# Kernel tuning notes

Hardware: AMD Instinct MI355X
Metric: run time of the kernel (lower is better)

The kernel has to match this reference:

```python
import jax, jax.numpy as jnp
import numpy as np

D_MODEL = 2048
N_HEADS = 16
D_HEAD = D_MODEL // N_HEADS  # 128
SEQ = 2048
BATCH = 2


def setup_inputs() -> dict:
    key = jax.random.key(0)
    ks = jax.random.split(key, 6)
    x = jax.random.normal(ks[0], (SEQ, BATCH, D_MODEL), dtype=jnp.float32)
    # Realistic RoPE angles: theta[t, i] = t / 10000^(2i/d_head)
    inv_freq = 1.0 / (10000.0 ** (jnp.arange(0, D_HEAD, 2, dtype=jnp.float32) / D_HEAD))
    freqs = jnp.outer(jnp.arange(SEQ, dtype=jnp.float32), inv_freq)  # (SEQ, D_HEAD/2)
    s = 1.0 / np.sqrt(D_MODEL)
    W_qkv = jax.random.normal(ks[1], (3 * D_MODEL, D_MODEL), dtype=jnp.float32) * s
    b_qkv = jax.random.normal(ks[2], (3 * D_MODEL,), dtype=jnp.float32) * 0.01
    W_o = jax.random.normal(ks[3], (D_MODEL, D_MODEL), dtype=jnp.float32) * s
    b_o = jax.random.normal(ks[4], (D_MODEL,), dtype=jnp.float32) * 0.01
    return {"x": x, "freqs": freqs, "W_qkv": W_qkv, "b_qkv": b_qkv, "W_o": W_o, "b_o": b_o}


def _apply_rope(t, cos, sin):
    # t: (S, B, H, D); cos/sin: (S, 1, 1, D/2). Pairs are interleaved (even, odd),
    # matching torch.view_as_complex on reshape(..., -1, 2).
    tr = t.reshape(*t.shape[:-1], D_HEAD // 2, 2)
    a, b = tr[..., 0], tr[..., 1]
    out = jnp.stack([a * cos - b * sin, a * sin + b * cos], axis=-1)
    return out.reshape(t.shape)


def reference(x, freqs, W_qkv, b_qkv, W_o, b_o):
    S, B, _ = x.shape
    qkv = jnp.einsum('sbd,ed->sbe', x, W_qkv) + b_qkv  # (S, B, 3*D_MODEL)
    q, k, v = jnp.split(qkv, 3, axis=-1)
    q = q.reshape(S, B, N_HEADS, D_HEAD)
    k = k.reshape(S, B, N_HEADS, D_HEAD)
    v = v.reshape(S, B, N_HEADS, D_HEAD)
    cos = jnp.cos(freqs)[:, None, None, :]
    sin = jnp.sin(freqs)[:, None, None, :]
    q = _apply_rope(q, cos, sin)
    k = _apply_rope(k, cos, sin)
    # (S, B, H, D) -> (B, H, S, D)
    q = q.transpose(1, 2, 0, 3)
    k = k.transpose(1, 2, 0, 3)
    v = v.transpose(1, 2, 0, 3)
    scale = 1.0 / np.sqrt(D_HEAD).astype(np.float32)
    scores = jnp.einsum('bhqd,bhkd->bhqk', q, k) * scale  # (B, H, S, S)
    causal = jnp.tril(jnp.ones((S, S), dtype=bool))
    scores = jnp.where(causal, scores, jnp.finfo(scores.dtype).min)
    attn = jax.nn.softmax(scores, axis=-1)
    out = jnp.einsum('bhqk,bhkd->bhqd', attn, v)  # (B, H, S, D)
    out = out.transpose(2, 0, 1, 3).reshape(S, B, D_MODEL)
    return jnp.einsum('sbd,ed->sbe', out, W_o) + b_o
```

## Files before the change

kernel.cpp:

```cpp
#include <hip/hip_runtime.h>

#define D_MODEL 2048
#define N_HEADS 16
#define D_HEAD 128
#define SEQ 2048
#define BATCH 2
#define M_ROWS (SEQ*BATCH)
#define QKV_N  (3*D_MODEL)
#define ATTN_SCALE 0.08838834764831845f

typedef __attribute__((ext_vector_type(8))) short short8v;
typedef __attribute__((ext_vector_type(4))) float float4v;
typedef __attribute__((ext_vector_type(2))) unsigned int uint2v;
typedef __attribute__((ext_vector_type(4))) unsigned int uint4v;
typedef unsigned short u16;
typedef unsigned int   u32;

__device__ __forceinline__ u16 f32_bf16_rne(float f) {
    u32 u = __float_as_uint(f);
    return (u16)((u + 0x7FFFu + ((u >> 16) & 1u)) >> 16);
}
__device__ __forceinline__ float bf16_f32(u16 h) {
    return __uint_as_float(((u32)h) << 16);
}

__device__ __forceinline__ void gll16(const void* g, void* l) {
    __builtin_amdgcn_global_load_lds(
        (const __attribute__((address_space(1))) void*)g,
        (__attribute__((address_space(3))) void*)l, 16, 0, 0);
}

__global__ __launch_bounds__(256) void split_tiles(
    const float* __restrict__ src, u16* __restrict__ H, u16* __restrict__ L,
    const int R)
{
    const int kt = blockIdx.x, rt = blockIdx.y, t = threadIdx.x;
#pragma unroll
    for (int i = 0; i < 2; ++i) {
        const int s = i*256 + t;
        const int r = s >> 2, sub = s & 3;
        const float* p = src + (size_t)(rt*128 + r)*D_MODEL + kt*32 + sub*8;
        float4 v0 = ((const float4*)p)[0];
        float4 v1 = ((const float4*)p)[1];
        float vv[8] = {v0.x, v0.y, v0.z, v0.w, v1.x, v1.y, v1.z, v1.w};
        u16 hh[8], ll[8];
#pragma unroll
        for (int j = 0; j < 8; ++j) {
            hh[j] = f32_bf16_rne(vv[j]);
            ll[j] = f32_bf16_rne(vv[j] - bf16_f32(hh[j]));
        }
        const size_t off = ((size_t)kt*R + rt*128 + r)*32 + sub*8;
        *(uint4*)&H[off] = *(uint4*)hh;
        *(uint4*)&L[off] = *(uint4*)ll;
    }
}

__device__ __forceinline__ void ps_mainloop(
    const u16* __restrict__ Ah, const u16* __restrict__ Al,
    const u16* __restrict__ Bh, const u16* __restrict__ Bl,
    const int Mrows, const int Nrows, const int m0, const int n0,
    u16* lds, float4v (&acc)[4][4])
{
    const int t = threadIdx.x;
    const int lane = t & 63, wave = t >> 6;
    const int l16 = lane & 15, lg = lane >> 4;
    const int wm = wave >> 1, wn = wave & 1;
    u16* LAh = lds;          u16* LAl = lds + 4096;
    u16* LBh = lds + 8192;   u16* LBl = lds + 12288;
    const int ch0 = wave * 2;

    for (int kt = 0; kt < 64; ++kt) {
        __syncthreads();
        const size_t aoff = ((size_t)kt*Mrows + m0)*32;
        const size_t boff = ((size_t)kt*Nrows + n0)*32;
#pragma unroll
        for (int i = 0; i < 2; ++i) {
            const int ch = ch0 + i;
            const int go = ch*512 + lane*8;
            gll16(Ah + aoff + go, &LAh[ch*512]);
            gll16(Al + aoff + go, &LAl[ch*512]);
            gll16(Bh + boff + go, &LBh[ch*512]);
            gll16(Bl + boff + go, &LBl[ch*512]);
        }
        __syncthreads();

        short8v bh[4], bl[4];
#pragma unroll
        for (int fn = 0; fn < 4; ++fn) {
            const int rb = (wn*64 + fn*16 + l16)*32 + lg*8;
            bh[fn] = *(const short8v*)&LBh[rb];
            bl[fn] = *(const short8v*)&LBl[rb];
        }
#pragma unroll
        for (int fm = 0; fm < 4; ++fm) {
            const int ra = (wm*64 + fm*16 + l16)*32 + lg*8;
            short8v ah = *(const short8v*)&LAh[ra];
            short8v al = *(const short8v*)&LAl[ra];
#pragma unroll
            for (int fn = 0; fn < 4; ++fn) {
                acc[fm][fn] = __builtin_amdgcn_mfma_f32_16x16x32_bf16(ah, bh[fn], acc[fm][fn], 0,0,0);
                acc[fm][fn] = __builtin_amdgcn_mfma_f32_16x16x32_bf16(ah, bl[fn], acc[fm][fn], 0,0,0);
                acc[fm][fn] = __builtin_amdgcn_mfma_f32_16x16x32_bf16(al, bh[fn], acc[fm][fn], 0,0,0);
            }
        }
    }
}

__global__ __launch_bounds__(256, 3) void qkv_ps(
    const u16* __restrict__ Xh, const u16* __restrict__ Xl,
    const u16* __restrict__ Wh, const u16* __restrict__ Wl,
    const float* __restrict__ bias, const float* __restrict__ freqs,
    u16* __restrict__ Qh, u16* __restrict__ Ql,
    u16* __restrict__ Kh, u16* __restrict__ Kl,
    u16* __restrict__ Vh, u16* __restrict__ Vl)
{
    __shared__ u16 lds[16384];
    const int m0 = blockIdx.x*128, n0 = blockIdx.y*128;
    float4v acc[4][4];
#pragma unroll
    for (int i = 0; i < 4; ++i)
#pragma unroll
        for (int j = 0; j < 4; ++j)
#pragma unroll
            for (int r = 0; r < 4; ++r) acc[i][j][r] = 0.f;

    ps_mainloop(Xh, Xl, Wh, Wl, M_ROWS, QKV_N, m0, n0, lds, acc);

    const int t = threadIdx.x;
    const int lane = t & 63, wave = t >> 6;
    const int l16 = lane & 15, lg = lane >> 4;
    const int wm = wave >> 1, wn = wave & 1;
    const int sec = n0 >> 11;
    u16* __restrict__ hb = (sec == 0) ? Qh : ((sec == 1) ? Kh : Vh);
    u16* __restrict__ lb = (sec == 0) ? Ql : ((sec == 1) ? Kl : Vl);
#pragma unroll
    for (int fn = 0; fn < 4; ++fn) {
        const int n = n0 + wn*64 + fn*16 + l16;
        const float bn = bias[n];
        const int d = n & 127, hd = (n >> 7) & 15;
#pragma unroll
        for (int fm = 0; fm < 4; ++fm) {
#pragma unroll
            for (int r = 0; r < 4; ++r) {
                const int mrow = m0 + wm*64 + fm*16 + lg*4 + r;
                const int s = mrow >> 1, bb = mrow & 1;
                float v = acc[fm][fn][r] + bn;
                float outv;
                if (sec == 2) {
                    outv = v;
                } else {
                    float partner = __shfl_xor(v, 1, 64);
                    float fr = freqs[(size_t)s * 64 + (d >> 1)];
                    float sn, cs;
                    sincosf(fr, &sn, &cs);
                    outv = (n & 1) ? (partner*sn + v*cs) : (v*cs - partner*sn);
                    if (sec == 0) outv *= ATTN_SCALE;
                }
                size_t off = (((size_t)(bb*N_HEADS + hd) * SEQ) + s) * D_HEAD + d;
                u16 h = f32_bf16_rne(outv);
                hb[off] = h;
                lb[off] = f32_bf16_rne(outv - bf16_f32(h));
            }
        }
    }
}

__global__ __launch_bounds__(256, 3) void out_ps(
    const u16* __restrict__ Aph, const u16* __restrict__ Apl,
    const u16* __restrict__ Wh, const u16* __restrict__ Wl,
    const float* __restrict__ bias, float* __restrict__ Out)
{
    __shared__ u16 lds[16384];
    const int m0 = blockIdx.x*128, n0 = blockIdx.y*128;
    float4v acc[4][4];
#pragma unroll
    for (int i = 0; i < 4; ++i)
#pragma unroll
        for (int j = 0; j < 4; ++j)
#pragma unroll
            for (int r = 0; r < 4; ++r) acc[i][j][r] = 0.f;

    ps_mainloop(Aph, Apl, Wh, Wl, M_ROWS, D_MODEL, m0, n0, lds, acc);

    const int t = threadIdx.x;
    const int lane = t & 63, wave = t >> 6;
    const int l16 = lane & 15, lg = lane >> 4;
    const int wm = wave >> 1, wn = wave & 1;
#pragma unroll
    for (int fn = 0; fn < 4; ++fn) {
        const int n = n0 + wn*64 + fn*16 + l16;
        const float bn = bias[n];
#pragma unroll
        for (int fm = 0; fm < 4; ++fm) {
#pragma unroll
            for (int r = 0; r < 4; ++r) {
                const int mrow = m0 + wm*64 + fm*16 + lg*4 + r;
                Out[(size_t)mrow * D_MODEL + n] = acc[fm][fn][r] + bn;
            }
        }
    }
}

#define STAGE_SPLIT(vv, sH, sL)                                              \
    {                                                                        \
        _Pragma("unroll")                                                    \
        for (int q = 0; q < 4; ++q) {                                        \
            float4 v = vv[q];                                                \
            int off = ((half*2 + (q>>1))*128 + row)*8 + (q&1)*4;             \
            u16 h0 = f32_bf16_rne(v.x), h1 = f32_bf16_rne(v.y),              \
                h2 = f32_bf16_rne(v.z), h3 = f32_bf16_rne(v.w);              \
            ushort4 hv = make_ushort4(h0, h1, h2, h3);                       \
            ushort4 lv = make_ushort4(f32_bf16_rne(v.x - bf16_f32(h0)),      \
                                      f32_bf16_rne(v.y - bf16_f32(h1)),      \
                                      f32_bf16_rne(v.z - bf16_f32(h2)),      \
                                      f32_bf16_rne(v.w - bf16_f32(h3)));     \
            *(ushort4*)&sH[off] = hv;                                        \
            *(ushort4*)&sL[off] = lv;                                        \
        }                                                                    \
    }

#define GEMM_PROLOGUE()                                                      \
    __shared__ u16 sAh[4*128*8], sAl[4*128*8], sBh[4*128*8], sBl[4*128*8];   \
    const int t = threadIdx.x;                                               \
    const int m0 = blockIdx.x * 128, n0 = blockIdx.y * 128;                  \
    const int row = t >> 1, half = t & 1;                                    \
    const int lane = t & 63, wave = t >> 6;                                  \
    const int wm = wave >> 1, wn = wave & 1;                                 \
    const int l16 = lane & 15, lg = lane >> 4;                               \
    float4v acc[4][4];                                                       \
    _Pragma("unroll")                                                        \
    for (int i = 0; i < 4; ++i)                                              \
        _Pragma("unroll")                                                    \
        for (int j = 0; j < 4; ++j)                                          \
            _Pragma("unroll")                                                 \
            for (int r = 0; r < 4; ++r) acc[i][j][r] = 0.f;

#define GEMM_MAINLOOP(Aptr, Bptr)                                            \
    const float* Arow = (Aptr) + (size_t)(m0 + row) * D_MODEL + half*16;     \
    const float* Brow = (Bptr) + (size_t)(n0 + row) * D_MODEL + half*16;     \
    float4 pa[4], pb[4];                                                     \
    _Pragma("unroll")                                                        \
    for (int q = 0; q < 4; ++q) {                                            \
        pa[q] = ((const float4*)Arow)[q];                                    \
        pb[q] = ((const float4*)Brow)[q];                                    \
    }                                                                        \
    for (int kt = 0; kt < D_MODEL/32; ++kt) {                                \
        if (kt) __syncthreads();                                             \
        STAGE_SPLIT(pa, sAh, sAl);                                           \
        STAGE_SPLIT(pb, sBh, sBl);                                           \
        if (kt < D_MODEL/32 - 1) {                                           \
            Arow += 32; Brow += 32;                                          \
            _Pragma("unroll")                                                \
            for (int q = 0; q < 4; ++q) {                                    \
                pa[q] = ((const float4*)Arow)[q];                            \
                pb[q] = ((const float4*)Brow)[q];                            \
            }                                                                \
        }                                                                    \
        __syncthreads();                                                     \
        const int abase = lg*128 + wm*64 + l16;                              \
        const int bbase = lg*128 + wn*64 + l16;                              \
        short8v bh[4], bl[4];                                                \
        _Pragma("unroll")                                                    \
        for (int fn = 0; fn < 4; ++fn) {                                     \
            bh[fn] = ((const short8v*)sBh)[bbase + fn*16];                   \
            bl[fn] = ((const short8v*)sBl)[bbase + fn*16];                   \
        }                                                                    \
        _Pragma("unroll")                                                    \
        for (int fm = 0; fm < 4; ++fm) {                                     \
            short8v ah = ((const short8v*)sAh)[abase + fm*16];               \
            short8v al = ((const short8v*)sAl)[abase + fm*16];               \
            _Pragma("unroll")                                                \
            for (int fn = 0; fn < 4; ++fn) {                                 \
                acc[fm][fn] = __builtin_amdgcn_mfma_f32_16x16x32_bf16(       \
                    ah, bh[fn], acc[fm][fn], 0, 0, 0);                       \
                acc[fm][fn] = __builtin_amdgcn_mfma_f32_16x16x32_bf16(       \
                    ah, bl[fn], acc[fm][fn], 0, 0, 0);                       \
                acc[fm][fn] = __builtin_amdgcn_mfma_f32_16x16x32_bf16(       \
                    al, bh[fn], acc[fm][fn], 0, 0, 0);                       \
            }                                                                \
        }                                                                    \
    }

__global__ __launch_bounds__(256, 2) void qkv_rope_mfma(
    const float* __restrict__ X, const float* __restrict__ W,
    const float* __restrict__ bias, const float* __restrict__ freqs,
    u16* __restrict__ Qh, u16* __restrict__ Ql,
    u16* __restrict__ Kh, u16* __restrict__ Kl,
    u16* __restrict__ Vh, u16* __restrict__ Vl)
{
    GEMM_PROLOGUE();
    GEMM_MAINLOOP(X, W);
    const int sec = n0 >> 11;
    u16* __restrict__ hb = (sec == 0) ? Qh : ((sec == 1) ? Kh : Vh);
    u16* __restrict__ lb = (sec == 0) ? Ql : ((sec == 1) ? Kl : Vl);
#pragma unroll
    for (int fn = 0; fn < 4; ++fn) {
        const int n = n0 + wn*64 + fn*16 + l16;
        const float bn = bias[n];
        const int d = n & 127, hd = (n >> 7) & 15;
#pragma unroll
        for (int fm = 0; fm < 4; ++fm) {
#pragma unroll
            for (int r = 0; r < 4; ++r) {
                const int mrow = m0 + wm*64 + fm*16 + lg*4 + r;
                const int s = mrow >> 1, bb = mrow & 1;
                float v = acc[fm][fn][r] + bn;
                float outv;
                if (sec == 2) {
                    outv = v;
                } else {
                    float partner = __shfl_xor(v, 1, 64);
                    float fr = freqs[(size_t)s * 64 + (d >> 1)];
                    float sn, cs;
                    sincosf(fr, &sn, &cs);
                    outv = (n & 1) ? (partner*sn + v*cs) : (v*cs - partner*sn);
                    if (sec == 0) outv *= ATTN_SCALE;
                }
                size_t off = (((size_t)(bb*N_HEADS + hd) * SEQ) + s) * D_HEAD + d;
                u16 h = f32_bf16_rne(outv);
                hb[off] = h;
                lb[off] = f32_bf16_rne(outv - bf16_f32(h));
            }
        }
    }
}

__global__ __launch_bounds__(256, 2) void out_proj_mfma(
    const float* __restrict__ A, const float* __restrict__ W,
    const float* __restrict__ bias, float* __restrict__ Out)
{
    GEMM_PROLOGUE();
    GEMM_MAINLOOP(A, W);
#pragma unroll
    for (int fn = 0; fn < 4; ++fn) {
        const int n = n0 + wn*64 + fn*16 + l16;
        const float bn = bias[n];
#pragma unroll
        for (int fm = 0; fm < 4; ++fm) {
#pragma unroll
            for (int r = 0; r < 4; ++r) {
                const int mrow = m0 + wm*64 + fm*16 + lg*4 + r;
                Out[(size_t)mrow * D_MODEL + n] = acc[fm][fn][r] + bn;
            }
        }
    }
}

#define QH_O 0
#define QL_O 8192
#define KH_O 16384
#define KL_O 20480
#define VH_O 24576
#define VL_O 28672

#define PV_DB(DB)                                                            \
    {                                                                        \
        uint2v th0, th1, tl0, tl1;                                           \
        u32 aH = vbH + DB*1024, aL = vbL + DB*1024;                          \
        asm volatile("ds_read_b64_tr_b16 %0, %4\n\t"                         \
                     "ds_read_b64_tr_b16 %1, %4 offset:128\n\t"              \
                     "ds_read_b64_tr_b16 %2, %5\n\t"                         \
                     "ds_read_b64_tr_b16 %3, %5 offset:128\n\t"              \
                     "s_waitcnt lgkmcnt(0)"                                  \
                     : "=v"(th0), "=v"(th1), "=v"(tl0), "=v"(tl1)            \
                     : "v"(aH), "v"(aL));                                    \
        __builtin_amdgcn_sched_barrier(0);                                   \
        uint4v uh; uh.x = th0.x; uh.y = th0.y; uh.z = th1.x; uh.w = th1.y;   \
        uint4v ul; ul.x = tl0.x; ul.y = tl0.y; ul.z = tl1.x; ul.w = tl1.y;   \
        short8v vfh = __builtin_bit_cast(short8v, uh);                       \
        short8v vfl = __builtin_bit_cast(short8v, ul);                       \
        o[DB] = __builtin_amdgcn_mfma_f32_16x16x32_bf16(vfh, pfh, o[DB], 0,0,0); \
        o[DB] = __builtin_amdgcn_mfma_f32_16x16x32_bf16(vfh, pfl, o[DB], 0,0,0); \
        o[DB] = __builtin_amdgcn_mfma_f32_16x16x32_bf16(vfl, pfh, o[DB], 0,0,0); \
    }

template<int MODE>
__global__ __launch_bounds__(256, 2) void attn_mfma_t(
    const u16* __restrict__ Qh_g, const u16* __restrict__ Ql_g,
    const u16* __restrict__ Kh_g, const u16* __restrict__ Kl_g,
    const u16* __restrict__ Vh_g, const u16* __restrict__ Vl_g,
    float* __restrict__ Op, u16* __restrict__ AH, u16* __restrict__ AL)
{
    __shared__ __align__(16) u16 lds[32768];

    const int t = threadIdx.x;
    const int lane = t & 63, wave = t >> 6;
    const int l16 = lane & 15, lg = lane >> 4;

    const int bid = blockIdx.x;
    const int bh = (bid & 7) * 4 + ((bid >> 3) >> 4);
    const int pairid = (bid >> 3) & 15;
    const size_t ho = (size_t)bh * SEQ * D_HEAD;

    const int skv = t >> 3;
    const int sdb = t & 7;

    const u32 ldsb = (u32)(uintptr_t)lds;
    const u32 vbH = ldsb + VH_O*2 + lg*256 + l16*8;
    const u32 vbL = ldsb + VL_O*2 + lg*256 + l16*8;

    for (int pass = 0; pass < 2; ++pass) {
        const int qb = pass ? (31 - pairid) : pairid;
        const int q0 = qb * 64;
        __syncthreads();
#pragma unroll
        for (int i = 0; i < 2; ++i) {
            int task = i*256 + t;
            int qr = task >> 3, db = task & 7;
            size_t gsrc = ho + (size_t)(q0 + qr)*128 + db*16;
            uint4 h0 = *(const uint4*)(Qh_g + gsrc);
            uint4 h1 = *(const uint4*)(Qh_g + gsrc + 8);
            uint4 L0 = *(const uint4*)(Ql_g + gsrc);
            uint4 L1 = *(const uint4*)(Ql_g + gsrc + 8);
            *(uint4*)&lds[QH_O + ((db*2  )*64 + qr)*8] = h0;
            *(uint4*)&lds[QH_O + ((db*2+1)*64 + qr)*8] = h1;
            *(uint4*)&lds[QL_O + ((db*2  )*64 + qr)*8] = L0;
            *(uint4*)&lds[QL_O + ((db*2+1)*64 + qr)*8] = L1;
        }
        __syncthreads();
        short8v qfh[4], qfl[4];
#pragma unroll
        for (int c = 0; c < 4; ++c) {
            int g = c*4 + lg;
            qfh[c] = *(const short8v*)&lds[QH_O + (g*64 + wave*16 + l16)*8];
            qfl[c] = *(const short8v*)&lds[QL_O + (g*64 + wave*16 + l16)*8];
        }

        float4v o[8];
#pragma unroll
        for (int db = 0; db < 8; ++db)
#pragma unroll
            for (int r = 0; r < 4; ++r) o[db][r] = 0.f;
        float m_s = -1e30f, l_s = 0.f;

        const int jjmax = 2*qb + 1;
        for (int jj = 0; jj <= jjmax; ++jj) {
            const int kv0 = jj * 32;
            __syncthreads();
            {
                size_t gk = ho + (size_t)(kv0 + skv)*128 + sdb*16;
                uint4 kh0 = *(const uint4*)(Kh_g + gk);
                uint4 kh1 = *(const uint4*)(Kh_g + gk + 8);
                uint4 kl0 = *(const uint4*)(Kl_g + gk);
                uint4 kl1 = *(const uint4*)(Kl_g + gk + 8);
                uint4 vh0 = *(const uint4*)(Vh_g + gk);
                uint4 vh1 = *(const uint4*)(Vh_g + gk + 8);
                uint4 vl0 = *(const uint4*)(Vl_g + gk);
                uint4 vl1 = *(const uint4*)(Vl_g + gk + 8);
                const int k7 = skv & 7;
                const int g0 = sdb*2, g1 = sdb*2 + 1;
                *(uint4*)&lds[KH_O + skv*128 + ((g0^k7)<<3)] = kh0;
                *(uint4*)&lds[KH_O + skv*128 + ((g1^k7)<<3)] = kh1;
                *(uint4*)&lds[KL_O + skv*128 + ((g0^k7)<<3)] = kl0;
                *(uint4*)&lds[KL_O + skv*128 + ((g1^k7)<<3)] = kl1;
                const int vreg = (sdb*8 + (skv>>2))*64 + (skv&3)*16;
                *(uint4*)&lds[VH_O + vreg]     = vh0;
                *(uint4*)&lds[VH_O + vreg + 8] = vh1;
                *(uint4*)&lds[VL_O + vreg]     = vl0;
                *(uint4*)&lds[VL_O + vreg + 8] = vl1;
            }
            __syncthreads();

            float4v s0 = {0.f,0.f,0.f,0.f}, s1 = {0.f,0.f,0.f,0.f};
#pragma unroll
            for (int c = 0; c < 4; ++c) {
                const int x0 = ((c*4 + lg) ^ (l16 & 7)) << 3;
                short8v kh0 = *(const short8v*)&lds[KH_O + l16*128 + x0];
                short8v kl0 = *(const short8v*)&lds[KL_O + l16*128 + x0];
                short8v kh1 = *(const short8v*)&lds[KH_O + (16+l16)*128 + x0];
                short8v kl1 = *(const short8v*)&lds[KL_O + (16+l16)*128 + x0];
                s0 = __builtin_amdgcn_mfma_f32_16x16x32_bf16(kh0, qfh[c], s0, 0,0,0);
                s0 = __builtin_amdgcn_mfma_f32_16x16x32_bf16(kh0, qfl[c], s0, 0,0,0);
                s0 = __builtin_amdgcn_mfma_f32_16x16x32_bf16(kl0, qfh[c], s0, 0,0,0);
                s1 = __builtin_amdgcn_mfma_f32_16x16x32_bf16(kh1, qfh[c], s1, 0,0,0);
                s1 = __builtin_amdgcn_mfma_f32_16x16x32_bf16(kh1, qfl[c], s1, 0,0,0);
                s1 = __builtin_amdgcn_mfma_f32_16x16x32_bf16(kl1, qfh[c], s1, 0,0,0);
            }

            const int qg = q0 + wave*16 + l16;
            if (jj >= 2*qb) {
#pragma unroll
                for (int r = 0; r < 4; ++r) {
                    if (kv0 + lg*4 + r > qg)      s0[r] = -1e30f;
                    if (kv0 + 16 + lg*4 + r > qg) s1[r] = -1e30f;
                }
            }

            float mx = fmaxf(fmaxf(fmaxf(s0[0], s0[1]), fmaxf(s0[2], s0[3])),
                             fmaxf(fmaxf(s1[0], s1[1]), fmaxf(s1[2], s1[3])));
            mx = fmaxf(mx, __shfl_xor(mx, 16, 64));
            mx = fmaxf(mx, __shfl_xor(mx, 32, 64));
            const float newm = fmaxf(m_s, mx);
            const float alpha = __expf(m_s - newm);
            m_s = newm;
            float pA[4], pB[4];
#pragma unroll
            for (int r = 0; r < 4; ++r) {
                pA[r] = __expf(s0[r] - newm);
                pB[r] = __expf(s1[r] - newm);
            }
            float rs = (pA[0]+pA[1]+pA[2]+pA[3]) + (pB[0]+pB[1]+pB[2]+pB[3]);
            rs += __shfl_xor(rs, 16, 64);
            rs += __shfl_xor(rs, 32, 64);
            l_s = l_s * alpha + rs;
#pragma unroll
            for (int db = 0; db < 8; ++db)
#pragma unroll
                for (int r = 0; r < 4; ++r) o[db][r] *= alpha;

            u16 ph[8], pl[8];
#pragma unroll
            for (int r = 0; r < 4; ++r) {
                float T1 = __shfl_xor(pA[r], 32, 64);
                float T2 = __shfl_xor(pB[r], 32, 64);
                float pv = (lg==0) ? T1 : (lg==1) ? pA[r] : (lg==2) ? pB[r] : T2;
                float Rv = __shfl_xor(pv, 16, 64);
                float X  = (lg==0) ? pA[r] : (lg==1) ? Rv : (lg==2) ? T2 : Rv;
                float Y  = (lg==0) ? Rv    : (lg==1) ? T1 : (lg==2) ? Rv : pB[r];
                u16 hx = f32_bf16_rne(X);
                ph[r]   = hx; pl[r]   = f32_bf16_rne(X - bf16_f32(hx));
                u16 hy = f32_bf16_rne(Y);
                ph[4+r] = hy; pl[4+r] = f32_bf16_rne(Y - bf16_f32(hy));
            }
            short8v pfh, pfl;
            pfh[0]=(short)ph[0]; pfh[1]=(short)ph[1]; pfh[2]=(short)ph[2]; pfh[3]=(short)ph[3];
            pfh[4]=(short)ph[4]; pfh[5]=(short)ph[5]; pfh[6]=(short)ph[6]; pfh[7]=(short)ph[7];
            pfl[0]=(short)pl[0]; pfl[1]=(short)pl[1]; pfl[2]=(short)pl[2]; pfl[3]=(short)pl[3];
            pfl[4]=(short)pl[4]; pfl[5]=(short)pl[5]; pfl[6]=(short)pl[6]; pfl[7]=(short)pl[7];

            PV_DB(0) PV_DB(1) PV_DB(2) PV_DB(3)
            PV_DB(4) PV_DB(5) PV_DB(6) PV_DB(7)
        }

        const int bb = bh >> 4, hh = bh & 15;
        const float inv = 1.0f / l_s;
        const int s_row = q0 + wave*16 + l16;
        if constexpr (MODE == 0) {
            float* orow = Op + (size_t)(s_row*BATCH + bb) * D_MODEL + hh*128;
#pragma unroll
            for (int tile = 0; tile < 8; ++tile) {
                float4 w = make_float4(o[tile][0]*inv, o[tile][1]*inv,
                                       o[tile][2]*inv, o[tile][3]*inv);
                *(float4*)(orow + tile*16 + lg*4) = w;
            }
        } else {
            const int m = s_row*BATCH + bb;
#pragma unroll
            for (int tile = 0; tile < 8; ++tile) {
                const int kt = hh*4 + (tile >> 1);
                const size_t off = ((size_t)kt*M_ROWS + m)*32 + (tile & 1)*16 + lg*4;
                u16 hh4[4], ll4[4];
#pragma unroll
                for (int r = 0; r < 4; ++r) {
                    float w = o[tile][r]*inv;
                    hh4[r] = f32_bf16_rne(w);
                    ll4[r] = f32_bf16_rne(w - bf16_f32(hh4[r]));
                }
                *(ushort4*)&AH[off] = make_ushort4(hh4[0], hh4[1], hh4[2], hh4[3]);
                *(ushort4*)&AL[off] = make_ushort4(ll4[0], ll4[1], ll4[2], ll4[3]);
            }
        }
    }
}

extern "C" void kernel_launch(void* const* d_in, const int* in_sizes, int n_in,
                              void* d_out, int out_size, void* d_ws, size_t ws_size,
                              hipStream_t stream) {
    const float* x      = (const float*)d_in[0];
    const float* freqs  = (const float*)d_in[1];
    const float* W_qkv  = (const float*)d_in[2];
    const float* b_qkv  = (const float*)d_in[3];
    const float* W_o    = (const float*)d_in[4];
    const float* b_o    = (const float*)d_in[5];
    float* out = (float*)d_out;

    const size_t PX = (size_t)M_ROWS * D_MODEL;
    const size_t PW = (size_t)QKV_N  * D_MODEL;
    const size_t PO = (size_t)D_MODEL* D_MODEL;
    u16* ws16 = (u16*)d_ws;

    if (ws_size >= (10*PX + 2*PW + 2*PO) * sizeof(u16)) {
        u16* Xh  = ws16;            u16* Xl  = Xh  + PX;
        u16* Wqh = Xl + PX;         u16* Wql = Wqh + PW;
        u16* Woh = Wql + PW;        u16* Wol = Woh + PO;
        u16* Qh  = Wol + PO;        u16* Ql  = Qh + PX;
        u16* Kh  = Ql + PX;         u16* Kl  = Kh + PX;
        u16* Vh  = Kl + PX;         u16* Vl  = Vh + PX;
        u16* Ahp = Vl + PX;         u16* Alp = Ahp + PX;

        split_tiles<<<dim3(64, M_ROWS/128), 256, 0, stream>>>(x,     Xh,  Xl,  M_ROWS);
        split_tiles<<<dim3(64, QKV_N/128),  256, 0, stream>>>(W_qkv, Wqh, Wql, QKV_N);
        split_tiles<<<dim3(64, D_MODEL/128),256, 0, stream>>>(W_o,   Woh, Wol, D_MODEL);
        qkv_ps<<<dim3(M_ROWS/128, QKV_N/128), 256, 0, stream>>>(
            Xh, Xl, Wqh, Wql, b_qkv, freqs, Qh, Ql, Kh, Kl, Vh, Vl);
        attn_mfma_t<1><<<dim3(512), 256, 0, stream>>>(
            Qh, Ql, Kh, Kl, Vh, Vl, nullptr, Ahp, Alp);
        out_ps<<<dim3(M_ROWS/128, D_MODEL/128), 256, 0, stream>>>(
            Ahp, Alp, Woh, Wol, b_o, out);
    } else {
        u16 *Qh = ws16,       *Ql = ws16 + PX,   *Kh = ws16 + 2*PX,
            *Kl = ws16 + 3*PX, *Vh = ws16 + 4*PX, *Vl = ws16 + 5*PX;
        float* attn = (float*)(ws16 + 6*PX);

        qkv_rope_mfma<<<dim3(M_ROWS/128, QKV_N/128), 256, 0, stream>>>(
            x, W_qkv, b_qkv, freqs, Qh, Ql, Kh, Kl, Vh, Vl);
        attn_mfma_t<0><<<dim3(512), 256, 0, stream>>>(
            Qh, Ql, Kh, Kl, Vh, Vl, attn, nullptr, nullptr);
        out_proj_mfma<<<dim3(M_ROWS/128, D_MODEL/128), 256, 0, stream>>>(
            attn, W_o, b_o, out);
    }
}
```

Before: 730.4 us.

## Double-buffer LDS in split-bf16 GEMMs and prefetch K/V tiles in attention

The shared GEMM mainloop now uses two LDS buffers. It issues the global-to-LDS loads for the next k-tile before computing the current one, replacing two barriers per iteration with one vmcnt wait and barrier at the end. The attention kernel prefetches the next K/V block into registers while the current block is written to LDS and computed. LDS per GEMM block doubles and launch bounds drop from 3 to 2 blocks per CU, trading occupancy for overlap. The fallback fp32-staging kernels and the small-workspace path are removed.

```diff
diff --git a/kernel.cpp b/kernel.cpp
--- a/kernel.cpp
+++ b/kernel.cpp
@@ -65,48 +65,74 @@
     const int lane = t & 63, wave = t >> 6;
     const int l16 = lane & 15, lg = lane >> 4;
     const int wm = wave >> 1, wn = wave & 1;
-    u16* LAh = lds;          u16* LAl = lds + 4096;
-    u16* LBh = lds + 8192;   u16* LBl = lds + 12288;
     const int ch0 = wave * 2;
 
-    for (int kt = 0; kt < 64; ++kt) {
-        __syncthreads();
-        const size_t aoff = ((size_t)kt*Mrows + m0)*32;
-        const size_t boff = ((size_t)kt*Nrows + n0)*32;
+    {
+        const size_t aoff = (size_t)m0 * 32;
+        const size_t boff = (size_t)n0 * 32;
 #pragma unroll
         for (int i = 0; i < 2; ++i) {
             const int ch = ch0 + i;
             const int go = ch*512 + lane*8;
-            gll16(Ah + aoff + go, &LAh[ch*512]);
-            gll16(Al + aoff + go, &LAl[ch*512]);
-            gll16(Bh + boff + go, &LBh[ch*512]);
-            gll16(Bl + boff + go, &LBl[ch*512]);
-        }
-        __syncthreads();
-
-        short8v bh[4], bl[4];
+            gll16(Ah + aoff + go, &lds[        ch*512]);
+            gll16(Al + aoff + go, &lds[ 4096 + ch*512]);
+            gll16(Bh + boff + go, &lds[ 8192 + ch*512]);
+            gll16(Bl + boff + go, &lds[12288 + ch*512]);
+        }
+    }
+    asm volatile("s_waitcnt vmcnt(0)" ::: "memory");
+    __builtin_amdgcn_s_barrier();
+    __builtin_amdgcn_sched_barrier(0);
+
+    int cur = 0;
+    for (int kt = 0; kt < 64; ++kt) {
+        if (kt < 63) {
+            u16* dst = lds + (cur^1)*16384;
+            const size_t aoff = ((size_t)(kt+1)*Mrows + m0)*32;
+            const size_t boff = ((size_t)(kt+1)*Nrows + n0)*32;
+#pragma unroll
+            for (int i = 0; i < 2; ++i) {
+                const int ch = ch0 + i;
+                const int go = ch*512 + lane*8;
+                gll16(Ah + aoff + go, &dst[        ch*512]);
+                gll16(Al + aoff + go, &dst[ 4096 + ch*512]);
+                gll16(Bh + boff + go, &dst[ 8192 + ch*512]);
+                gll16(Bl + boff + go, &dst[12288 + ch*512]);
+            }
+        }
+        const u16* src = lds + cur*16384;
+        short8v bhf[4], blf[4], ahf[4], alf[4];
 #pragma unroll
         for (int fn = 0; fn < 4; ++fn) {
             const int rb = (wn*64 + fn*16 + l16)*32 + lg*8;
-            bh[fn] = *(const short8v*)&LBh[rb];
-            bl[fn] = *(const short8v*)&LBl[rb];
+            bhf[fn] = *(const short8v*)&src[ 8192 + rb];
+            blf[fn] = *(const short8v*)&src[12288 + rb];
         }
 #pragma unroll
         for (int fm = 0; fm < 4; ++fm) {
             const int ra = (wm*64 + fm*16 + l16)*32 + lg*8;
-            short8v ah = *(const short8v*)&LAh[ra];
-            short8v al = *(const short8v*)&LAl[ra];
+            ahf[fm] = *(const short8v*)&src[       ra];
+            alf[fm] = *(const short8v*)&src[4096 + ra];
+        }
+        asm volatile("s_waitcnt lgkmcnt(0)" ::: "memory");
+        __builtin_amdgcn_sched_barrier(0);
+#pragma unroll
+        for (int fm = 0; fm < 4; ++fm) {
 #pragma unroll
             for (int fn = 0; fn < 4; ++fn) {
-                acc[fm][fn] = __builtin_amdgcn_mfma_f32_16x16x32_bf16(ah, bh[fn], acc[fm][fn], 0,0,0);
-                acc[fm][fn] = __builtin_amdgcn_mfma_f32_16x16x32_bf16(ah, bl[fn], acc[fm][fn], 0,0,0);
-                acc[fm][fn] = __builtin_amdgcn_mfma_f32_16x16x32_bf16(al, bh[fn], acc[fm][fn], 0,0,0);
-            }
-        }
-    }
-}
-
-__global__ __launch_bounds__(256, 3) void qkv_ps(
+                acc[fm][fn] = __builtin_amdgcn_mfma_f32_16x16x32_bf16(ahf[fm], bhf[fn], acc[fm][fn], 0,0,0);
+                acc[fm][fn] = __builtin_amdgcn_mfma_f32_16x16x32_bf16(ahf[fm], blf[fn], acc[fm][fn], 0,0,0);
+                acc[fm][fn] = __builtin_amdgcn_mfma_f32_16x16x32_bf16(alf[fm], bhf[fn], acc[fm][fn], 0,0,0);
+            }
+        }
+        asm volatile("s_waitcnt vmcnt(0)" ::: "memory");
+        __builtin_amdgcn_s_barrier();
+        __builtin_amdgcn_sched_barrier(0);
+        cur ^= 1;
+    }
+}
+
+__global__ __launch_bounds__(256, 2) void qkv_ps(
     const u16* __restrict__ Xh, const u16* __restrict__ Xl,
     const u16* __restrict__ Wh, const u16* __restrict__ Wl,
     const float* __restrict__ bias, const float* __restrict__ freqs,
@@ -114,7 +140,7 @@
     u16* __restrict__ Kh, u16* __restrict__ Kl,
     u16* __restrict__ Vh, u16* __restrict__ Vl)
 {
-    __shared__ u16 lds[16384];
+    __shared__ u16 lds[32768];
     const int m0 = blockIdx.x*128, n0 = blockIdx.y*128;
     float4v acc[4][4];
 #pragma unroll
@@ -165,12 +191,12 @@
     }
 }
 
-__global__ __launch_bounds__(256, 3) void out_ps(
+__global__ __launch_bounds__(256, 2) void out_ps(
     const u16* __restrict__ Aph, const u16* __restrict__ Apl,
     const u16* __restrict__ Wh, const u16* __restrict__ Wl,
     const float* __restrict__ bias, float* __restrict__ Out)
 {
-    __shared__ u16 lds[16384];
+    __shared__ u16 lds[32768];
     const int m0 = blockIdx.x*128, n0 = blockIdx.y*128;
     float4v acc[4][4];
 #pragma unroll
@@ -186,151 +212,6 @@
     const int lane = t & 63, wave = t >> 6;
     const int l16 = lane & 15, lg = lane >> 4;
     const int wm = wave >> 1, wn = wave & 1;
-#pragma unroll
-    for (int fn = 0; fn < 4; ++fn) {
-        const int n = n0 + wn*64 + fn*16 + l16;
-        const float bn = bias[n];
-#pragma unroll
-        for (int fm = 0; fm < 4; ++fm) {
-#pragma unroll
-            for (int r = 0; r < 4; ++r) {
-                const int mrow = m0 + wm*64 + fm*16 + lg*4 + r;
-                Out[(size_t)mrow * D_MODEL + n] = acc[fm][fn][r] + bn;
-            }
-        }
-    }
-}
-
-#define STAGE_SPLIT(vv, sH, sL)                                              \
-    {                                                                        \
-        _Pragma("unroll")                                                    \
-        for (int q = 0; q < 4; ++q) {                                        \
-            float4 v = vv[q];                                                \
-            int off = ((half*2 + (q>>1))*128 + row)*8 + (q&1)*4;             \
-            u16 h0 = f32_bf16_rne(v.x), h1 = f32_bf16_rne(v.y),              \
-                h2 = f32_bf16_rne(v.z), h3 = f32_bf16_rne(v.w);              \
-            ushort4 hv = make_ushort4(h0, h1, h2, h3);                       \
-            ushort4 lv = make_ushort4(f32_bf16_rne(v.x - bf16_f32(h0)),      \
-                                      f32_bf16_rne(v.y - bf16_f32(h1)),      \
-                                      f32_bf16_rne(v.z - bf16_f32(h2)),      \
-                                      f32_bf16_rne(v.w - bf16_f32(h3)));     \
-            *(ushort4*)&sH[off] = hv;                                        \
-            *(ushort4*)&sL[off] = lv;                                        \
-        }                                                                    \
-    }
-
-#define GEMM_PROLOGUE()                                                      \
-    __shared__ u16 sAh[4*128*8], sAl[4*128*8], sBh[4*128*8], sBl[4*128*8];   \
-    const int t = threadIdx.x;                                               \
-    const int m0 = blockIdx.x * 128, n0 = blockIdx.y * 128;                  \
-    const int row = t >> 1, half = t & 1;                                    \
-    const int lane = t & 63, wave = t >> 6;                                  \
-    const int wm = wave >> 1, wn = wave & 1;                                 \
-    const int l16 = lane & 15, lg = lane >> 4;                               \
-    float4v acc[4][4];                                                       \
-    _Pragma("unroll")                                                        \
-    for (int i = 0; i < 4; ++i)                                              \
-        _Pragma("unroll")                                                    \
-        for (int j = 0; j < 4; ++j)                                          \
-            _Pragma("unroll")                                                 \
-            for (int r = 0; r < 4; ++r) acc[i][j][r] = 0.f;
-
-#define GEMM_MAINLOOP(Aptr, Bptr)                                            \
-    const float* Arow = (Aptr) + (size_t)(m0 + row) * D_MODEL + half*16;     \
-    const float* Brow = (Bptr) + (size_t)(n0 + row) * D_MODEL + half*16;     \
-    float4 pa[4], pb[4];                                                     \
-    _Pragma("unroll")                                                        \
-    for (int q = 0; q < 4; ++q) {                                            \
-        pa[q] = ((const float4*)Arow)[q];                                    \
-        pb[q] = ((const float4*)Brow)[q];                                    \
-    }                                                                        \
-    for (int kt = 0; kt < D_MODEL/32; ++kt) {                                \
-        if (kt) __syncthreads();                                             \
-        STAGE_SPLIT(pa, sAh, sAl);                                           \
-        STAGE_SPLIT(pb, sBh, sBl);                                           \
-        if (kt < D_MODEL/32 - 1) {                                           \
-            Arow += 32; Brow += 32;                                          \
-            _Pragma("unroll")                                                \
-            for (int q = 0; q < 4; ++q) {                                    \
-                pa[q] = ((const float4*)Arow)[q];                            \
-                pb[q] = ((const float4*)Brow)[q];                            \
-            }                                                                \
-        }                                                                    \
-        __syncthreads();                                                     \
-        const int abase = lg*128 + wm*64 + l16;                              \
-        const int bbase = lg*128 + wn*64 + l16;                              \
-        short8v bh[4], bl[4];                                                \
-        _Pragma("unroll")                                                    \
-        for (int fn = 0; fn < 4; ++fn) {                                     \
-            bh[fn] = ((const short8v*)sBh)[bbase + fn*16];                   \
-            bl[fn] = ((const short8v*)sBl)[bbase + fn*16];                   \
-        }                                                                    \
-        _Pragma("unroll")                                                    \
-        for (int fm = 0; fm < 4; ++fm) {                                     \
-            short8v ah = ((const short8v*)sAh)[abase + fm*16];               \
-            short8v al = ((const short8v*)sAl)[abase + fm*16];               \
-            _Pragma("unroll")                                                \
-            for (int fn = 0; fn < 4; ++fn) {                                 \
-                acc[fm][fn] = __builtin_amdgcn_mfma_f32_16x16x32_bf16(       \
-                    ah, bh[fn], acc[fm][fn], 0, 0, 0);                       \
-                acc[fm][fn] = __builtin_amdgcn_mfma_f32_16x16x32_bf16(       \
-                    ah, bl[fn], acc[fm][fn], 0, 0, 0);                       \
-                acc[fm][fn] = __builtin_amdgcn_mfma_f32_16x16x32_bf16(       \
-                    al, bh[fn], acc[fm][fn], 0, 0, 0);                       \
-            }                                                                \
-        }                                                                    \
-    }
-
-__global__ __launch_bounds__(256, 2) void qkv_rope_mfma(
-    const float* __restrict__ X, const float* __restrict__ W,
-    const float* __restrict__ bias, const float* __restrict__ freqs,
-    u16* __restrict__ Qh, u16* __restrict__ Ql,
-    u16* __restrict__ Kh, u16* __restrict__ Kl,
-    u16* __restrict__ Vh, u16* __restrict__ Vl)
-{
-    GEMM_PROLOGUE();
-    GEMM_MAINLOOP(X, W);
-    const int sec = n0 >> 11;
-    u16* __restrict__ hb = (sec == 0) ? Qh : ((sec == 1) ? Kh : Vh);
-    u16* __restrict__ lb = (sec == 0) ? Ql : ((sec == 1) ? Kl : Vl);
-#pragma unroll
-    for (int fn = 0; fn < 4; ++fn) {
-        const int n = n0 + wn*64 + fn*16 + l16;
-        const float bn = bias[n];
-        const int d = n & 127, hd = (n >> 7) & 15;
-#pragma unroll
-        for (int fm = 0; fm < 4; ++fm) {
-#pragma unroll
-            for (int r = 0; r < 4; ++r) {
-                const int mrow = m0 + wm*64 + fm*16 + lg*4 + r;
-                const int s = mrow >> 1, bb = mrow & 1;
-                float v = acc[fm][fn][r] + bn;
-                float outv;
-                if (sec == 2) {
-                    outv = v;
-                } else {
-                    float partner = __shfl_xor(v, 1, 64);
-                    float fr = freqs[(size_t)s * 64 + (d >> 1)];
-                    float sn, cs;
-                    sincosf(fr, &sn, &cs);
-                    outv = (n & 1) ? (partner*sn + v*cs) : (v*cs - partner*sn);
-                    if (sec == 0) outv *= ATTN_SCALE;
-                }
-                size_t off = (((size_t)(bb*N_HEADS + hd) * SEQ) + s) * D_HEAD + d;
-                u16 h = f32_bf16_rne(outv);
-                hb[off] = h;
-                lb[off] = f32_bf16_rne(outv - bf16_f32(h));
-            }
-        }
-    }
-}
-
-__global__ __launch_bounds__(256, 2) void out_proj_mfma(
-    const float* __restrict__ A, const float* __restrict__ W,
-    const float* __restrict__ bias, float* __restrict__ Out)
-{
-    GEMM_PROLOGUE();
-    GEMM_MAINLOOP(A, W);
 #pragma unroll
     for (int fn = 0; fn < 4; ++fn) {
         const int n = n0 + wn*64 + fn*16 + l16;
@@ -374,12 +255,11 @@
         o[DB] = __builtin_amdgcn_mfma_f32_16x16x32_bf16(vfl, pfh, o[DB], 0,0,0); \
     }
 
-template<int MODE>
-__global__ __launch_bounds__(256, 2) void attn_mfma_t(
+__global__ __launch_bounds__(256, 2) void attn_mfma(
     const u16* __restrict__ Qh_g, const u16* __restrict__ Ql_g,
     const u16* __restrict__ Kh_g, const u16* __restrict__ Kl_g,
     const u16* __restrict__ Vh_g, const u16* __restrict__ Vl_g,
-    float* __restrict__ Op, u16* __restrict__ AH, u16* __restrict__ AL)
+    u16* __restrict__ AH, u16* __restrict__ AL)
 {
     __shared__ __align__(16) u16 lds[32768];
 
@@ -398,6 +278,33 @@
     const u32 ldsb = (u32)(uintptr_t)lds;
     const u32 vbH = ldsb + VH_O*2 + lg*256 + l16*8;
     const u32 vbL = ldsb + VL_O*2 + lg*256 + l16*8;
+
+    uint4 kh0, kh1, kl0, kl1, vh0, vh1, vl0, vl1;
+
+    auto kvload = [&](int kvb) {
+        size_t gk = ho + (size_t)(kvb*32 + skv)*128 + sdb*16;
+        kh0 = *(const uint4*)(Kh_g + gk);
+        kh1 = *(const uint4*)(Kh_g + gk + 8);
+        kl0 = *(const uint4*)(Kl_g + gk);
+        kl1 = *(const uint4*)(Kl_g + gk + 8);
+        vh0 = *(const uint4*)(Vh_g + gk);
+        vh1 = *(const uint4*)(Vh_g + gk + 8);
+        vl0 = *(const uint4*)(Vl_g + gk);
+        vl1 = *(const uint4*)(Vl_g + gk + 8);
+    };
+    auto kvwrite = [&]() {
+        const int k7 = skv & 7;
+        const int g0 = sdb*2, g1 = sdb*2 + 1;
+        *(uint4*)&lds[KH_O + skv*128 + ((g0^k7)<<3)] = kh0;
+        *(uint4*)&lds[KH_O + skv*128 + ((g1^k7)<<3)] = kh1;
+        *(uint4*)&lds[KL_O + skv*128 + ((g0^k7)<<3)] = kl0;
+        *(uint4*)&lds[KL_O + skv*128 + ((g1^k7)<<3)] = kl1;
+        const int vreg = (sdb*8 + (skv>>2))*64 + (skv&3)*16;
+        *(uint4*)&lds[VH_O + vreg]     = vh0;
+        *(uint4*)&lds[VH_O + vreg + 8] = vh1;
+        *(uint4*)&lds[VL_O + vreg]     = vl0;
+        *(uint4*)&lds[VL_O + vreg + 8] = vl1;
+    };
 
     for (int pass = 0; pass < 2; ++pass) {
         const int qb = pass ? (31 - pairid) : pairid;
@@ -426,6 +333,8 @@
             qfl[c] = *(const short8v*)&lds[QL_O + (g*64 + wave*16 + l16)*8];
         }
 
+        kvload(0);
+
         float4v o[8];
 #pragma unroll
         for (int db = 0; db < 8; ++db)
@@ -437,44 +346,26 @@
         for (int jj = 0; jj <= jjmax; ++jj) {
             const int kv0 = jj * 32;
             __syncthreads();
-            {
-                size_t gk = ho + (size_t)(kv0 + skv)*128 + sdb*16;
-                uint4 kh0 = *(const uint4*)(Kh_g + gk);
-                uint4 kh1 = *(const uint4*)(Kh_g + gk + 8);
-                uint4 kl0 = *(const uint4*)(Kl_g + gk);
-                uint4 kl1 = *(const uint4*)(Kl_g + gk + 8);
-                uint4 vh0 = *(const uint4*)(Vh_g + gk);
-                uint4 vh1 = *(const uint4*)(Vh_g + gk + 8);
-                uint4 vl0 = *(const uint4*)(Vl_g + gk);
-                uint4 vl1 = *(const uint4*)(Vl_g + gk + 8);
-                const int k7 = skv & 7;
-                const int g0 = sdb*2, g1 = sdb*2 + 1;
-                *(uint4*)&lds[KH_O + skv*128 + ((g0^k7)<<3)] = kh0;
-                *(uint4*)&lds[KH_O + skv*128 + ((g1^k7)<<3)] = kh1;
-                *(uint4*)&lds[KL_O + skv*128 + ((g0^k7)<<3)] = kl0;
-                *(uint4*)&lds[KL_O + skv*128 + ((g1^k7)<<3)] = kl1;
-                const int vreg = (sdb*8 + (skv>>2))*64 + (skv&3)*16;
-                *(uint4*)&lds[VH_O + vreg]     = vh0;
-                *(uint4*)&lds[VH_O + vreg + 8] = vh1;
-                *(uint4*)&lds[VL_O + vreg]     = vl0;
-                *(uint4*)&lds[VL_O + vreg + 8] = vl1;
-            }
-            __syncthreads();
+            kvwrite();
+            if (jj < jjmax) kvload(jj + 1);
+            asm volatile("s_waitcnt lgkmcnt(0)" ::: "memory");
+            __builtin_amdgcn_s_barrier();
+            __builtin_amdgcn_sched_barrier(0);
 
             float4v s0 = {0.f,0.f,0.f,0.f}, s1 = {0.f,0.f,0.f,0.f};
 #pragma unroll
             for (int c = 0; c < 4; ++c) {
                 const int x0 = ((c*4 + lg) ^ (l16 & 7)) << 3;
-                short8v kh0 = *(const short8v*)&lds[KH_O + l16*128 + x0];
-                short8v kl0 = *(const short8v*)&lds[KL_O + l16*128 + x0];
-                short8v kh1 = *(const short8v*)&lds[KH_O + (16+l16)*128 + x0];
-                short8v kl1 = *(const short8v*)&lds[KL_O + (16+l16)*128 + x0];
-                s0 = __builtin_amdgcn_mfma_f32_16x16x32_bf16(kh0, qfh[c], s0, 0,0,0);
-                s0 = __builtin_amdgcn_mfma_f32_16x16x32_bf16(kh0, qfl[c], s0, 0,0,0);
-                s0 = __builtin_amdgcn_mfma_f32_16x16x32_bf16(kl0, qfh[c], s0, 0,0,0);
-                s1 = __builtin_amdgcn_mfma_f32_16x16x32_bf16(kh1, qfh[c], s1, 0,0,0);
-                s1 = __builtin_amdgcn_mfma_f32_16x16x32_bf16(kh1, qfl[c], s1, 0,0,0);
-                s1 = __builtin_amdgcn_mfma_f32_16x16x32_bf16(kl1, qfh[c], s1, 0,0,0);
+                short8v K_h0 = *(const short8v*)&lds[KH_O + l16*128 + x0];
+                short8v K_l0 = *(const short8v*)&lds[KL_O + l16*128 + x0];
+                short8v K_h1 = *(const short8v*)&lds[KH_O + (16+l16)*128 + x0];
+                short8v K_l1 = *(const short8v*)&lds[KL_O + (16+l16)*128 + x0];
+                s0 = __builtin_amdgcn_mfma_f32_16x16x32_bf16(K_h0, qfh[c], s0, 0,0,0);
+                s0 = __builtin_amdgcn_mfma_f32_16x16x32_bf16(K_h0, qfl[c], s0, 0,0,0);
+                s0 = __builtin_amdgcn_mfma_f32_16x16x32_bf16(K_l0, qfh[c], s0, 0,0,0);
+                s1 = __builtin_amdgcn_mfma_f32_16x16x32_bf16(K_h1, qfh[c], s1, 0,0,0);
+                s1 = __builtin_amdgcn_mfma_f32_16x16x32_bf16(K_h1, qfl[c], s1, 0,0,0);
+                s1 = __builtin_amdgcn_mfma_f32_16x16x32_bf16(K_l1, qfh[c], s1, 0,0,0);
             }
 
             const int qg = q0 + wave*16 + l16;
@@ -535,30 +426,20 @@
         const int bb = bh >> 4, hh = bh & 15;
         const float inv = 1.0f / l_s;
         const int s_row = q0 + wave*16 + l16;
-        if constexpr (MODE == 0) {
-            float* orow = Op + (size_t)(s_row*BATCH + bb) * D_MODEL + hh*128;
-#pragma unroll
-            for (int tile = 0; tile < 8; ++tile) {
-                float4 w = make_float4(o[tile][0]*inv, o[tile][1]*inv,
-                                       o[tile][2]*inv, o[tile][3]*inv);
-                *(float4*)(orow + tile*16 + lg*4) = w;
-            }
-        } else {
-            const int m = s_row*BATCH + bb;
-#pragma unroll
-            for (int tile = 0; tile < 8; ++tile) {
-                const int kt = hh*4 + (tile >> 1);
-                const size_t off = ((size_t)kt*M_ROWS + m)*32 + (tile & 1)*16 + lg*4;
-                u16 hh4[4], ll4[4];
-#pragma unroll
-                for (int r = 0; r < 4; ++r) {
-                    float w = o[tile][r]*inv;
-                    hh4[r] = f32_bf16_rne(w);
-                    ll4[r] = f32_bf16_rne(w - bf16_f32(hh4[r]));
-                }
-                *(ushort4*)&AH[off] = make_ushort4(hh4[0], hh4[1], hh4[2], hh4[3]);
-                *(ushort4*)&AL[off] = make_ushort4(ll4[0], ll4[1], ll4[2], ll4[3]);
-            }
+        const int m = s_row*BATCH + bb;
+#pragma unroll
+        for (int tile = 0; tile < 8; ++tile) {
+            const int kt = hh*4 + (tile >> 1);
+            const size_t off = ((size_t)kt*M_ROWS + m)*32 + (tile & 1)*16 + lg*4;
+            u16 hh4[4], ll4[4];
+#pragma unroll
+            for (int r = 0; r < 4; ++r) {
+                float w = o[tile][r]*inv;
+                hh4[r] = f32_bf16_rne(w);
+                ll4[r] = f32_bf16_rne(w - bf16_f32(hh4[r]));
+            }
+            *(ushort4*)&AH[off] = make_ushort4(hh4[0], hh4[1], hh4[2], hh4[3]);
+            *(ushort4*)&AL[off] = make_ushort4(ll4[0], ll4[1], ll4[2], ll4[3]);
         }
     }
 }
@@ -579,34 +460,20 @@
     const size_t PO = (size_t)D_MODEL* D_MODEL;
     u16* ws16 = (u16*)d_ws;
 
-    if (ws_size >= (10*PX + 2*PW + 2*PO) * sizeof(u16)) {
-        u16* Xh  = ws16;            u16* Xl  = Xh  + PX;
-        u16* Wqh = Xl + PX;         u16* Wql = Wqh + PW;
-        u16* Woh = Wql + PW;        u16* Wol = Woh + PO;
-        u16* Qh  = Wol + PO;        u16* Ql  = Qh + PX;
-        u16* Kh  = Ql + PX;         u16* Kl  = Kh + PX;
-        u16* Vh  = Kl + PX;         u16* Vl  = Vh + PX;
-        u16* Ahp = Vl + PX;         u16* Alp = Ahp + PX;
-
-        split_tiles<<<dim3(64, M_ROWS/128), 256, 0, stream>>>(x,     Xh,  Xl,  M_ROWS);
-        split_tiles<<<dim3(64, QKV_N/128),  256, 0, stream>>>(W_qkv, Wqh, Wql, QKV_N);
-        split_tiles<<<dim3(64, D_MODEL/128),256, 0, stream>>>(W_o,   Woh, Wol, D_MODEL);
-        qkv_ps<<<dim3(M_ROWS/128, QKV_N/128), 256, 0, stream>>>(
-            Xh, Xl, Wqh, Wql, b_qkv, freqs, Qh, Ql, Kh, Kl, Vh, Vl);
-        attn_mfma_t<1><<<dim3(512), 256, 0, stream>>>(
-            Qh, Ql, Kh, Kl, Vh, Vl, nullptr, Ahp, Alp);
-        out_ps<<<dim3(M_ROWS/128, D_MODEL/128), 256, 0, stream>>>(
-            Ahp, Alp, Woh, Wol, b_o, out);
-    } else {
-        u16 *Qh = ws16,       *Ql = ws16 + PX,   *Kh = ws16 + 2*PX,
-            *Kl = ws16 + 3*PX, *Vh = ws16 + 4*PX, *Vl = ws16 + 5*PX;
-        float* attn = (float*)(ws16 + 6*PX);
-
-        qkv_rope_mfma<<<dim3(M_ROWS/128, QKV_N/128), 256, 0, stream>>>(
-            x, W_qkv, b_qkv, freqs, Qh, Ql, Kh, Kl, Vh, Vl);
-        attn_mfma_t<0><<<dim3(512), 256, 0, stream>>>(
-            Qh, Ql, Kh, Kl, Vh, Vl, attn, nullptr, nullptr);
-        out_proj_mfma<<<dim3(M_ROWS/128, D_MODEL/128), 256, 0, stream>>>(
-            attn, W_o, b_o, out);
-    }
-}
+    u16* Xh  = ws16;            u16* Xl  = Xh  + PX;
+    u16* Wqh = Xl + PX;         u16* Wql = Wqh + PW;
+    u16* Woh = Wql + PW;        u16* Wol = Woh + PO;
+    u16* Qh  = Wol + PO;        u16* Ql  = Qh + PX;
+    u16* Kh  = Ql + PX;         u16* Kl  = Kh + PX;
+    u16* Vh  = Kl + PX;         u16* Vl  = Vh + PX;
+    u16* Ahp = Vl + PX;         u16* Alp = Ahp + PX;
+
+    split_tiles<<<dim3(64, M_ROWS/128), 256, 0, stream>>>(x,     Xh,  Xl,  M_ROWS);
+    split_tiles<<<dim3(64, QKV_N/128),  256, 0, stream>>>(W_qkv, Wqh, Wql, QKV_N);
+    split_tiles<<<dim3(64, D_MODEL/128),256, 0, stream>>>(W_o,   Woh, Wol, D_MODEL);
+    qkv_ps<<<dim3(M_ROWS/128, QKV_N/128), 256, 0, stream>>>(
+        Xh, Xl, Wqh, Wql, b_qkv, freqs, Qh, Ql, Kh, Kl, Vh, Vl);
+    attn_mfma<<<dim3(512), 256, 0, stream>>>(Qh, Ql, Kh, Kl, Vh, Vl, Ahp, Alp);
+    out_ps<<<dim3(M_ROWS/128, D_MODEL/128), 256, 0, stream>>>(
+        Ahp, Alp, Woh, Wol, b_o, out);
+}
```

Measured after the change: 768.4 us. +5.2%, slower.
